# Kernel optimization log

Hardware: AMD Instinct MI355X
Metric: run time of the kernel (lower is better)

## Reference

```python
import jax, jax.numpy as jnp
import numpy as np

B, T, H, D = 1, 2048, 32, 64
SCALE = 0.015625  # 1/64 = 1/head_size
DEG = 2


def setup_inputs() -> dict:
    key = jax.random.key(0)
    k1, k2, k3, k4 = jax.random.split(key, 4)
    q = jax.random.normal(k1, (B, T, H, D), dtype=jnp.float32)
    k = jax.random.normal(k2, (B, T, H, D), dtype=jnp.float32)
    v = jax.random.normal(k3, (B, T, H, D), dtype=jnp.float32)
    # log_G: per-token, per-head log decay (must be <= 0)
    g = -0.1 * jax.random.uniform(k4, (B, T, H), dtype=jnp.float32)
    return {"q": q, "k": k, "v": v, "g": g}


def reference(q, k, v, g):
    # q,k,v: [B,T,H,D]; g: [B,T,H] log-decay (log_G)
    # Power retention, deg=2, attention (quadratic) form for T <= switch_over_seq_len.
    g_cum = jnp.cumsum(g, axis=1)                         # [B,T,H]
    gc = jnp.transpose(g_cum, (0, 2, 1))                  # [B,H,T]
    # decay weight exp(gc[t]-gc[s]) for s<=t, 0 otherwise
    log_decay = gc[:, :, :, None] - gc[:, :, None, :]     # [B,H,T,S]
    causal = jnp.tril(jnp.ones((T, T), dtype=bool))
    decay = jnp.where(causal, jnp.exp(log_decay), 0.0)    # [B,H,T,S]
    qk = jnp.einsum("bthd,bshd->bhts", q, k) * SCALE      # [B,H,T,S]
    w = (qk ** DEG) * decay                               # nonneg scores, deg=2
    num = jnp.einsum("bhts,bshd->bthd", w, v)             # [B,T,H,D]
    denom = jnp.transpose(w.sum(-1), (0, 2, 1))           # [B,T,H]
    out = num / jnp.maximum(denom, 1.0)[..., None]
    return out
```

## Files before the change

kernel.cpp:

```cpp
#include <hip/hip_runtime.h>

#define T_DIM 2048
#define H_DIM 32
#define D_DIM 64
#define SCALE_F 0.015625f
#define ROWSTRIDE 2048

typedef unsigned short ushort;
typedef __attribute__((ext_vector_type(8))) short short8;
typedef __attribute__((ext_vector_type(16))) float f32x16;
typedef __attribute__((ext_vector_type(2))) float f32x2;
typedef __attribute__((ext_vector_type(4))) float f32x4;

#define MFMA32(A, B, C) __builtin_amdgcn_mfma_f32_32x32x16_bf16((A), (B), (C), 0, 0, 0)

__global__ __launch_bounds__(256)
void cumsum_g_kernel(const float* __restrict__ g, float* __restrict__ gc) {
    const int h = blockIdx.x;
    const int tid = threadIdx.x;
    const int PER = T_DIM / 256;

    __shared__ float sums[256];

    float loc[8];
    float run = 0.f;
    const int t0 = tid * PER;
    for (int i = 0; i < PER; ++i) {
        run += g[(size_t)(t0 + i) * H_DIM + h];
        loc[i] = run;
    }
    sums[tid] = run;
    __syncthreads();

    for (int off = 1; off < 256; off <<= 1) {
        float vv = (tid >= off) ? sums[tid - off] : 0.f;
        __syncthreads();
        sums[tid] += vv;
        __syncthreads();
    }
    float excl = (tid == 0) ? 0.f : sums[tid - 1];

    for (int i = 0; i < PER; ++i)
        gc[(size_t)h * T_DIM + t0 + i] = excl + loc[i];
}

__device__ __forceinline__ short8 ld8(const ushort* p) {
    return *reinterpret_cast<const short8*>(p);
}

__device__ __forceinline__ unsigned cvt_pk_bf16(float lo, float hi) {
    unsigned r;
    asm("v_cvt_pk_bf16_f32 %0, %1, %2" : "=v"(r) : "v"(lo), "v"(hi));
    return r;
}

__device__ __forceinline__ short8 pack_w2(const f32x2* w2) {
    unsigned p0 = cvt_pk_bf16(w2[0][0], w2[0][1]);
    unsigned p1 = cvt_pk_bf16(w2[1][0], w2[1][1]);
    unsigned p2 = cvt_pk_bf16(w2[2][0], w2[2][1]);
    unsigned p3 = cvt_pk_bf16(w2[3][0], w2[3][1]);
    asm("v_permlane32_swap_b32 %0, %1" : "+v"(p0), "+v"(p2));
    asm("v_permlane32_swap_b32 %0, %1" : "+v"(p1), "+v"(p3));
    union { unsigned u[4]; short8 s; } af;
    af.u[0] = p0; af.u[1] = p1; af.u[2] = p2; af.u[3] = p3;
    return af.s;
}

template<int MODE>
__device__ __forceinline__ void unit32(
    const ushort* ldsK, const ushort* ldsV,
    int lofs, int hi, int l31,
    const short8 (&qr)[4], f32x16& o0, f32x16& o1, f32x2& den2)
{
    const short8 kf0 = ld8(ldsK + lofs);
    const short8 kf1 = ld8(ldsK + 512 + lofs);
    const short8 kf2 = ld8(ldsK + 1024 + lofs);
    const short8 kf3 = ld8(ldsK + 1536 + lofs);
    const short8 vf0 = ld8(ldsV + lofs);
    const short8 vf1 = ld8(ldsV + 512 + lofs);
    const short8 vf2 = ld8(ldsV + 1024 + lofs);
    const short8 vf3 = ld8(ldsV + 1536 + lofs);

    f32x16 c;
#pragma unroll
    for (int i = 0; i < 16; ++i) c[i] = 0.f;
    c = MFMA32(kf0, qr[0], c);
    c = MFMA32(kf1, qr[1], c);
    c = MFMA32(kf2, qr[2], c);
    c = MFMA32(kf3, qr[3], c);

    f32x2 w2[8];
#pragma unroll
    for (int i = 0; i < 8; ++i) {
        const int r0 = 2 * i;
        f32x2 x; x[0] = c[r0]; x[1] = c[r0 + 1];
        f32x2 ww = x * x;
        if (MODE == 1) {
            const int sl0 = (r0 & 3) + 8 * (r0 >> 2) + 4 * hi;
            ww[0] = (sl0 <= l31) ? ww[0] : 0.f;
            ww[1] = (sl0 + 1 <= l31) ? ww[1] : 0.f;
        }
        w2[i] = ww;
        den2 += ww;
    }
    const short8 a0 = pack_w2(&w2[0]);
    o0 = MFMA32(a0, vf0, o0);
    o1 = MFMA32(a0, vf2, o1);
    const short8 a1 = pack_w2(&w2[4]);
    o0 = MFMA32(a1, vf1, o0);
    o1 = MFMA32(a1, vf3, o1);
}

struct KStage { f32x4 a, b; float g; };
struct VStage { float v0, v1, v2, v3, v4, v5, v6, v7; };

__device__ __forceinline__ void issue_k(KStage& s, const float* kg,
                                        const float* gch, int s0, int tid) {
    const int r  = tid >> 3;
    const int d0 = (tid & 7) * 8;
    const float* p = kg + (size_t)(s0 + r) * ROWSTRIDE + d0;
    s.a = *reinterpret_cast<const f32x4*>(p);
    s.b = *reinterpret_cast<const f32x4*>(p + 4);
    s.g = gch[s0 + r];
}

__device__ __forceinline__ void write_k(const KStage& s, ushort* bufK, int tid) {
    const int r  = tid >> 3;
    const int ks = (tid & 7) >> 1;
    const int hh = tid & 1;
    const float ek = __expf(-0.5f * s.g);
    union { unsigned u[4]; short8 s8; } o;
    o.u[0] = cvt_pk_bf16(s.a[0] * ek, s.a[1] * ek);
    o.u[1] = cvt_pk_bf16(s.a[2] * ek, s.a[3] * ek);
    o.u[2] = cvt_pk_bf16(s.b[0] * ek, s.b[1] * ek);
    o.u[3] = cvt_pk_bf16(s.b[2] * ek, s.b[3] * ek);
    *reinterpret_cast<short8*>(bufK + (r >> 5) * 2048 + ks * 512 + hh * 256
                               + (r & 31) * 8) = o.s8;
}

__device__ __forceinline__ void issue_v(VStage& s, const float* vg, int s0, int tid) {
    const int c = tid >> 5, l31 = tid & 31;
    const int tile = c >> 3, dblk = (c >> 2) & 1, kh2 = (c >> 1) & 1, hiv = c & 1;
    const int tb = s0 + tile * 32 + kh2 * 16 + hiv * 8;
    const float* p = vg + (size_t)tb * ROWSTRIDE + dblk * 32 + l31;
    s.v0 = p[0 * ROWSTRIDE]; s.v1 = p[1 * ROWSTRIDE];
    s.v2 = p[2 * ROWSTRIDE]; s.v3 = p[3 * ROWSTRIDE];
    s.v4 = p[4 * ROWSTRIDE]; s.v5 = p[5 * ROWSTRIDE];
    s.v6 = p[6 * ROWSTRIDE]; s.v7 = p[7 * ROWSTRIDE];
}

__device__ __forceinline__ void write_v(const VStage& s, ushort* bufV, int tid) {
    const int c = tid >> 5, l31 = tid & 31;
    const int tile = c >> 3;
    const int c3 = c & 7;
    union { unsigned u[4]; short8 s8; } o;
    o.u[0] = cvt_pk_bf16(s.v0, s.v1);
    o.u[1] = cvt_pk_bf16(s.v2, s.v3);
    o.u[2] = cvt_pk_bf16(s.v4, s.v5);
    o.u[3] = cvt_pk_bf16(s.v6, s.v7);
    *reinterpret_cast<short8*>(bufV + tile * 2048 + c3 * 256 + l31 * 8) = o.s8;
}

__global__ __launch_bounds__(512, 4)
void retention_fused_kernel(const float* __restrict__ q,
                            const float* __restrict__ k,
                            const float* __restrict__ v,
                            const float* __restrict__ gc,
                            float* __restrict__ out) {
    __shared__ ushort buf[2][8192];
    __shared__ float pmd[8 * 32];

    const int bid = blockIdx.x;
    const int h   = bid & 31;
    const int QB  = 15 - (bid >> 5);

    const int tid = threadIdx.x;
    const int w   = tid >> 6;
    const int qi  = w & 3;
    const int si  = w >> 2;
    const int lane = tid & 63;
    const int hi  = lane >> 5;
    const int l31 = lane & 31;
    const int lofs = hi * 256 + l31 * 8;
    const int myT32 = 4 * QB + qi;

    const float* gch = gc + (size_t)h * T_DIM;
    const float* kg  = k + h * 64;
    const float* vg  = v + h * 64;

    short8 qr[4];
    {
        const int t = myT32 * 32 + l31;
        const float eq = SCALE_F * __expf(0.5f * gch[t]);
        const float* qrow = q + (size_t)t * ROWSTRIDE + h * 64 + hi * 8;
#pragma unroll
        for (int ks = 0; ks < 4; ++ks) {
            f32x4 fa = *reinterpret_cast<const f32x4*>(qrow + ks * 16);
            f32x4 fb = *reinterpret_cast<const f32x4*>(qrow + ks * 16 + 4);
            union { unsigned u[4]; short8 s8; } o;
            o.u[0] = cvt_pk_bf16(fa[0] * eq, fa[1] * eq);
            o.u[1] = cvt_pk_bf16(fa[2] * eq, fa[3] * eq);
            o.u[2] = cvt_pk_bf16(fb[0] * eq, fb[1] * eq);
            o.u[3] = cvt_pk_bf16(fb[2] * eq, fb[3] * eq);
            qr[ks] = o.s8;
        }
    }

    f32x16 o0, o1;
#pragma unroll
    for (int i = 0; i < 16; ++i) { o0[i] = 0.f; o1[i] = 0.f; }
    f32x2 d2; d2[0] = 0.f; d2[1] = 0.f;

    const int NJ = 2 * QB + 2;

    KStage kst; VStage vst;
    issue_k(kst, kg, gch, 0, tid);
    issue_v(vst, vg, 0, tid);
    write_k(kst, buf[0], tid);
    write_v(vst, buf[0] + 4096, tid);
    __syncthreads();

    for (int J = 0; J < NJ; ++J) {
        const int cur = J & 1;
        if (J + 1 < NJ) {
            issue_k(kst, kg, gch, (J + 1) * 64, tid);
            issue_v(vst, vg, (J + 1) * 64, tid);
        }
        const ushort* bK = buf[cur];
        const ushort* bV = buf[cur] + 4096;
        const int c1 = 2 * J + si;

        if (c1 < myT32)
            unit32<0>(bK + si * 2048, bV + si * 2048, lofs, hi, l31, qr, o0, o1, d2);
        else if (c1 == myT32)
            unit32<1>(bK + si * 2048, bV + si * 2048, lofs, hi, l31, qr, o0, o1, d2);

        if (J + 1 < NJ) {
            write_k(kst, buf[cur ^ 1], tid);
            write_v(vst, buf[cur ^ 1] + 4096, tid);
        }
        __syncthreads();
    }

    float* pm = (float*)&buf[0][0];

    float den = d2[0] + d2[1];
    den += __shfl_xor(den, 32);
    if (hi == 0) pmd[(qi * 2 + si) * 32 + l31] = den;

    if (si == 0) {
#pragma unroll
        for (int rr = 0; rr < 16; ++rr) {
            const int row = (rr & 3) + 8 * (rr >> 2) + 4 * hi;
            pm[(qi * 32 + row) * 64 + l31]      = o0[rr];
            pm[(qi * 32 + row) * 64 + 32 + l31] = o1[rr];
        }
    }
    __syncthreads();
    if (si == 1) {
#pragma unroll
        for (int rr = 0; rr < 16; ++rr) {
            const int row = (rr & 3) + 8 * (rr >> 2) + 4 * hi;
            pm[(qi * 32 + row) * 64 + l31]      += o0[rr];
            pm[(qi * 32 + row) * 64 + 32 + l31] += o1[rr];
        }
    }
    __syncthreads();

    {
        const int row  = tid >> 2;
        const int qq   = row >> 5;
        const int r32  = row & 31;
        const int dseg = (tid & 3) * 16;
        const float dtot = pmd[(qq * 2 + 0) * 32 + r32]
                         + pmd[(qq * 2 + 1) * 32 + r32];
        const float inv = 1.f / fmaxf(dtot, 1.f);
        const float* src = pm + (qq * 32 + r32) * 64 + dseg;
        float* dst = out + ((size_t)(QB * 128 + row) * H_DIM + h) * 64 + dseg;
#pragma unroll
        for (int jv = 0; jv < 4; ++jv) {
            f32x4 s = *reinterpret_cast<const f32x4*>(src + 4 * jv);
            s *= inv;
            *reinterpret_cast<f32x4*>(dst + 4 * jv) = s;
        }
    }
}

extern "C" void kernel_launch(void* const* d_in, const int* in_sizes, int n_in,
                              void* d_out, int out_size, void* d_ws, size_t ws_size,
                              hipStream_t stream) {
    const float* q = (const float*)d_in[0];
    const float* k = (const float*)d_in[1];
    const float* v = (const float*)d_in[2];
    const float* g = (const float*)d_in[3];
    float* out = (float*)d_out;

    float* gc = (float*)d_ws;

    cumsum_g_kernel<<<H_DIM, 256, 0, stream>>>(g, gc);
    retention_fused_kernel<<<512, 512, 0, stream>>>(q, k, v, gc, out);
}
```

Measured before the change: 50.05 us.

## Double KV tile per iteration to 128 rows and XOR-swizzle LDS layout

Each main-loop iteration now stages 128 key/value rows instead of 64. Every wave therefore processes two 32-row subtiles per barrier, which halves the number of __syncthreads and loop iterations. The K and V LDS writes and reads use an XOR swizzle on the 16-byte chunk index to spread accesses across banks and avoid conflicts. The cost is doubled LDS use (64KB total) and more staging registers per thread, which may lower occupancy.

New measurement: 105.0 us. 110% more time.

```diff
diff --git a/kernel.cpp b/kernel.cpp
--- a/kernel.cpp
+++ b/kernel.cpp
@@ -69,17 +69,18 @@
 template<int MODE>
 __device__ __forceinline__ void unit32(
     const ushort* ldsK, const ushort* ldsV,
-    int lofs, int hi, int l31,
+    const int (&loK)[4], const int (&loV)[4],
+    int hi, int l31,
     const short8 (&qr)[4], f32x16& o0, f32x16& o1, f32x2& den2)
 {
-    const short8 kf0 = ld8(ldsK + lofs);
-    const short8 kf1 = ld8(ldsK + 512 + lofs);
-    const short8 kf2 = ld8(ldsK + 1024 + lofs);
-    const short8 kf3 = ld8(ldsK + 1536 + lofs);
-    const short8 vf0 = ld8(ldsV + lofs);
-    const short8 vf1 = ld8(ldsV + 512 + lofs);
-    const short8 vf2 = ld8(ldsV + 1024 + lofs);
-    const short8 vf3 = ld8(ldsV + 1536 + lofs);
+    const short8 kf0 = ld8(ldsK + loK[0]);
+    const short8 kf1 = ld8(ldsK + loK[1]);
+    const short8 kf2 = ld8(ldsK + loK[2]);
+    const short8 kf3 = ld8(ldsK + loK[3]);
+    const short8 vf0 = ld8(ldsV + loV[0]);
+    const short8 vf1 = ld8(ldsV + loV[1]);
+    const short8 vf2 = ld8(ldsV + loV[2]);
+    const short8 vf3 = ld8(ldsV + loV[3]);
 
     f32x16 c;
 #pragma unroll
@@ -111,36 +112,39 @@
     o1 = MFMA32(a1, vf3, o1);
 }
 
-struct KStage { f32x4 a, b; float g; };
-struct VStage { float v0, v1, v2, v3, v4, v5, v6, v7; };
-
-__device__ __forceinline__ void issue_k(KStage& s, const float* kg,
-                                        const float* gch, int s0, int tid) {
-    const int r  = tid >> 3;
-    const int d0 = (tid & 7) * 8;
+struct KS { f32x4 a, b; float g; };
+struct VS { float v0, v1, v2, v3, v4, v5, v6, v7; };
+
+__device__ __forceinline__ void issue_k(KS& s, const float* kg,
+                                        const float* gch, int s0, int slot) {
+    const int r  = slot >> 3;
+    const int d0 = (slot & 7) * 8;
     const float* p = kg + (size_t)(s0 + r) * ROWSTRIDE + d0;
     s.a = *reinterpret_cast<const f32x4*>(p);
     s.b = *reinterpret_cast<const f32x4*>(p + 4);
     s.g = gch[s0 + r];
 }
 
-__device__ __forceinline__ void write_k(const KStage& s, ushort* bufK, int tid) {
-    const int r  = tid >> 3;
-    const int ks = (tid & 7) >> 1;
-    const int hh = tid & 1;
+__device__ __forceinline__ void write_k(const KS& s, ushort* bufK, int slot) {
+    const int r  = slot >> 3;
+    const int ks = (slot & 7) >> 1;
+    const int hh = slot & 1;
     const float ek = __expf(-0.5f * s.g);
     union { unsigned u[4]; short8 s8; } o;
     o.u[0] = cvt_pk_bf16(s.a[0] * ek, s.a[1] * ek);
     o.u[1] = cvt_pk_bf16(s.a[2] * ek, s.a[3] * ek);
     o.u[2] = cvt_pk_bf16(s.b[0] * ek, s.b[1] * ek);
     o.u[3] = cvt_pk_bf16(s.b[2] * ek, s.b[3] * ek);
-    *reinterpret_cast<short8*>(bufK + (r >> 5) * 2048 + ks * 512 + hh * 256
-                               + (r & 31) * 8) = o.s8;
-}
-
-__device__ __forceinline__ void issue_v(VStage& s, const float* vg, int s0, int tid) {
-    const int c = tid >> 5, l31 = tid & 31;
-    const int tile = c >> 3, dblk = (c >> 2) & 1, kh2 = (c >> 1) & 1, hiv = c & 1;
+    const int chunk = (r >> 5) * 256 + ks * 64 + hh * 32
+                    + ((r & 31) ^ (2 * ks + hh));
+    *reinterpret_cast<short8*>(bufK + chunk * 8) = o.s8;
+}
+
+__device__ __forceinline__ void issue_v(VS& s, const float* vg, int s0, int slot) {
+    const int c = slot >> 5;
+    const int l31 = slot & 31;
+    const int tile = c >> 3, c3 = c & 7;
+    const int dblk = c3 >> 2, kh2 = (c3 >> 1) & 1, hiv = c3 & 1;
     const int tb = s0 + tile * 32 + kh2 * 16 + hiv * 8;
     const float* p = vg + (size_t)tb * ROWSTRIDE + dblk * 32 + l31;
     s.v0 = p[0 * ROWSTRIDE]; s.v1 = p[1 * ROWSTRIDE];
@@ -149,16 +153,16 @@
     s.v6 = p[6 * ROWSTRIDE]; s.v7 = p[7 * ROWSTRIDE];
 }
 
-__device__ __forceinline__ void write_v(const VStage& s, ushort* bufV, int tid) {
-    const int c = tid >> 5, l31 = tid & 31;
-    const int tile = c >> 3;
-    const int c3 = c & 7;
+__device__ __forceinline__ void write_v(const VS& s, ushort* bufV, int slot) {
+    const int c = slot >> 5, l31 = slot & 31;
+    const int tile = c >> 3, c3 = c & 7;
     union { unsigned u[4]; short8 s8; } o;
     o.u[0] = cvt_pk_bf16(s.v0, s.v1);
     o.u[1] = cvt_pk_bf16(s.v2, s.v3);
     o.u[2] = cvt_pk_bf16(s.v4, s.v5);
     o.u[3] = cvt_pk_bf16(s.v6, s.v7);
-    *reinterpret_cast<short8*>(bufV + tile * 2048 + c3 * 256 + l31 * 8) = o.s8;
+    const int chunk = tile * 256 + c3 * 32 + (l31 ^ c3);
+    *reinterpret_cast<short8*>(bufV + chunk * 8) = o.s8;
 }
 
 __global__ __launch_bounds__(512, 4)
@@ -167,8 +171,7 @@
                             const float* __restrict__ v,
                             const float* __restrict__ gc,
                             float* __restrict__ out) {
-    __shared__ ushort buf[2][8192];
-    __shared__ float pmd[8 * 32];
+    __shared__ ushort buf[2][16384];
 
     const int bid = blockIdx.x;
     const int h   = bid & 31;
@@ -181,8 +184,17 @@
     const int lane = tid & 63;
     const int hi  = lane >> 5;
     const int l31 = lane & 31;
-    const int lofs = hi * 256 + l31 * 8;
     const int myT32 = 4 * QB + qi;
+
+    int loK[4], loV[4];
+#pragma unroll
+    for (int ks = 0; ks < 4; ++ks)
+        loK[ks] = (ks * 64 + hi * 32 + (l31 ^ (2 * ks + hi))) * 8;
+#pragma unroll
+    for (int m = 0; m < 4; ++m) {
+        const int c3 = (m >> 1) * 4 + (m & 1) * 2 + hi;
+        loV[m] = (c3 * 32 + (l31 ^ c3)) * 8;
+    }
 
     const float* gch = gc + (size_t)h * T_DIM;
     const float* kg  = k + h * 64;
@@ -211,38 +223,54 @@
     for (int i = 0; i < 16; ++i) { o0[i] = 0.f; o1[i] = 0.f; }
     f32x2 d2; d2[0] = 0.f; d2[1] = 0.f;
 
-    const int NJ = 2 * QB + 2;
-
-    KStage kst; VStage vst;
-    issue_k(kst, kg, gch, 0, tid);
-    issue_v(vst, vg, 0, tid);
-    write_k(kst, buf[0], tid);
-    write_v(vst, buf[0] + 4096, tid);
+    const int NJ = QB + 1;
+
+    KS k0s, k1s; VS v0s, v1s;
+    issue_k(k0s, kg, gch, 0, tid);
+    issue_k(k1s, kg, gch, 0, tid + 512);
+    issue_v(v0s, vg, 0, tid);
+    issue_v(v1s, vg, 0, tid + 512);
+    write_k(k0s, buf[0], tid);
+    write_k(k1s, buf[0], tid + 512);
+    write_v(v0s, buf[0] + 8192, tid);
+    write_v(v1s, buf[0] + 8192, tid + 512);
     __syncthreads();
 
     for (int J = 0; J < NJ; ++J) {
         const int cur = J & 1;
         if (J + 1 < NJ) {
-            issue_k(kst, kg, gch, (J + 1) * 64, tid);
-            issue_v(vst, vg, (J + 1) * 64, tid);
+            const int s0n = (J + 1) * 128;
+            issue_k(k0s, kg, gch, s0n, tid);
+            issue_k(k1s, kg, gch, s0n, tid + 512);
+            issue_v(v0s, vg, s0n, tid);
+            issue_v(v1s, vg, s0n, tid + 512);
         }
         const ushort* bK = buf[cur];
-        const ushort* bV = buf[cur] + 4096;
-        const int c1 = 2 * J + si;
+        const ushort* bV = buf[cur] + 8192;
+        const int c1 = 4 * J + 2 * si;
+        const int sub1 = 2 * si, sub2 = 2 * si + 1;
 
         if (c1 < myT32)
-            unit32<0>(bK + si * 2048, bV + si * 2048, lofs, hi, l31, qr, o0, o1, d2);
+            unit32<0>(bK + sub1 * 2048, bV + sub1 * 2048, loK, loV, hi, l31, qr, o0, o1, d2);
         else if (c1 == myT32)
-            unit32<1>(bK + si * 2048, bV + si * 2048, lofs, hi, l31, qr, o0, o1, d2);
+            unit32<1>(bK + sub1 * 2048, bV + sub1 * 2048, loK, loV, hi, l31, qr, o0, o1, d2);
+
+        if (c1 + 1 < myT32)
+            unit32<0>(bK + sub2 * 2048, bV + sub2 * 2048, loK, loV, hi, l31, qr, o0, o1, d2);
+        else if (c1 + 1 == myT32)
+            unit32<1>(bK + sub2 * 2048, bV + sub2 * 2048, loK, loV, hi, l31, qr, o0, o1, d2);
 
         if (J + 1 < NJ) {
-            write_k(kst, buf[cur ^ 1], tid);
-            write_v(vst, buf[cur ^ 1] + 4096, tid);
+            write_k(k0s, buf[cur ^ 1], tid);
+            write_k(k1s, buf[cur ^ 1], tid + 512);
+            write_v(v0s, buf[cur ^ 1] + 8192, tid);
+            write_v(v1s, buf[cur ^ 1] + 8192, tid + 512);
         }
         __syncthreads();
     }
 
-    float* pm = (float*)&buf[0][0];
+    float* pm  = (float*)&buf[0][0];
+    float* pmd = (float*)&buf[1][0];
 
     float den = d2[0] + d2[1];
     den += __shfl_xor(den, 32);
```
